# Optimization experiments

Hardware: AMD Instinct MI355X
Metric: run time of the kernel (lower is better)

Reference implementation:

```python
import jax, jax.numpy as jnp
import numpy as np

NUM_HEADS = 12
HEAD_SIZE = 64
HIDDEN = NUM_HEADS * HEAD_SIZE  # 768
ONE_SIDED_WINDOW = 256          # attention_window 512 // 2
NEG = -10000.0


def setup_inputs() -> dict:
    key = jax.random.key(0)
    ks = jax.random.split(key, 16)
    B, W, E, H = 1, 2048, 128, HIDDEN
    std = 0.02
    def lin(kw, kb):
        return (jax.random.normal(kw, (H, H), jnp.float32) * std,
                jax.random.normal(kb, (H,), jnp.float32) * std)
    q_w, q_b = lin(ks[0], ks[1])
    k_w, k_b = lin(ks[2], ks[3])
    v_w, v_b = lin(ks[4], ks[5])
    w2e_w, w2e_b = lin(ks[6], ks[7])
    e2w_w, e2w_b = lin(ks[8], ks[9])
    e2e_w, e2e_b = lin(ks[10], ks[11])
    return {
        "word_hidden_states": jax.random.normal(ks[12], (B, W, H), jnp.float32),
        "entity_hidden_states": jax.random.normal(ks[13], (B, E, H), jnp.float32),
        "attention_mask": jnp.zeros((B, 1, 1, W + E), jnp.float32),
        "q_w": q_w, "q_b": q_b, "k_w": k_w, "k_b": k_b, "v_w": v_w, "v_b": v_b,
        "w2e_w": w2e_w, "w2e_b": w2e_b, "e2w_w": e2w_w, "e2w_b": e2w_b,
        "e2e_w": e2e_w, "e2e_b": e2e_b,
    }


def reference(word_hidden_states, entity_hidden_states, attention_mask,
              q_w, q_b, k_w, k_b, v_w, v_b,
              w2e_w, w2e_b, e2w_w, e2w_b, e2e_w, e2e_b):
    B, W, H = word_hidden_states.shape
    E = entity_hidden_states.shape[1]
    S = W + E

    def heads(x):  # [B, L, H] -> [B, nh, L, hd]
        return x.reshape(B, -1, NUM_HEADS, HEAD_SIZE).transpose(0, 2, 1, 3)

    concat = jnp.concatenate([word_hidden_states, entity_hidden_states], axis=1)
    k = heads(concat @ k_w + k_b)          # [B, nh, S, hd]
    v = heads(concat @ v_w + v_b)
    q_w2w = heads(word_hidden_states @ q_w + q_b)
    q_w2e = heads(word_hidden_states @ w2e_w + w2e_b)
    q_e2w = heads(entity_hidden_states @ e2w_w + e2w_b)
    q_e2e = heads(entity_hidden_states @ e2e_w + e2e_b)

    k_word, k_ent = k[:, :, :W], k[:, :, W:]

    # --- w2w: Longformer sliding-window QK^T, then _conversion to a dense
    # [B, nh, W, W] matrix with out-of-band entries set to -10000. ---
    w2w = jnp.einsum('bhid,bhjd->bhij', q_w2w, k_word)  # [B, nh, W, W]
    idx = jnp.arange(W)
    in_band = jnp.abs(idx[:, None] - idx[None, :]) <= ONE_SIDED_WINDOW  # [W, W]
    # diagonal mask: float_mask[j] (-10000 where attention_mask != 0) added
    # within the band (broadcast over heads / query positions)
    mask_words = attention_mask[:, 0, 0, :W]                # [B, W]
    float_mask = jnp.where(mask_words != 0.0, NEG, 0.0)     # [B, W]
    w2w = w2w + float_mask[:, None, None, :]
    # _conversion: out-of-band -> -10000; also exact zeros -> -10000 (source quirk)
    w2w = jnp.where(in_band[None, None] & (w2w != 0.0), w2w, NEG)

    # --- entity-aware dense blocks ---
    w2e = jnp.einsum('bhid,bhjd->bhij', q_w2e, k_ent)    # [B, nh, W, E]
    e2w = jnp.einsum('bhid,bhjd->bhij', q_e2w, k_word)   # [B, nh, E, W]
    e2e = jnp.einsum('bhid,bhjd->bhij', q_e2e, k_ent)    # [B, nh, E, E]

    word_scores = jnp.concatenate([w2w, w2e], axis=3)    # [B, nh, W, S]
    ent_scores = jnp.concatenate([e2w, e2e], axis=3)     # [B, nh, E, S]
    scores = jnp.concatenate([word_scores, ent_scores], axis=2)  # [B, nh, S, S]

    scores = scores / jnp.sqrt(jnp.float32(HEAD_SIZE)) + attention_mask
    probs = jax.nn.softmax(scores, axis=-1)

    ctx = jnp.einsum('bhij,bhjd->bhid', probs, v)        # [B, nh, S, hd]
    ctx = ctx.transpose(0, 2, 1, 3).reshape(B, S, H)
    return ctx[:, :W, :], ctx[:, W:, :]
```

## Files before the change

kernel.cpp:

```cpp
#include <hip/hip_runtime.h>

typedef __bf16 bf16x8 __attribute__((ext_vector_type(8)));
typedef unsigned short u16x8 __attribute__((ext_vector_type(8)));
typedef u16x8 u16x8_a __attribute__((may_alias));
typedef unsigned int u32x2 __attribute__((ext_vector_type(2)));
typedef u32x2 u32x2_a __attribute__((may_alias));
typedef unsigned int u32x4 __attribute__((ext_vector_type(4)));
typedef u32x4 u32x4_a __attribute__((may_alias));
typedef float f32x4 __attribute__((ext_vector_type(4)));

#define LOG2E 1.4426950408889634f
#define NEGV  -10000.0f

__device__ __forceinline__ unsigned short f2bf(float f){
  union{float f; unsigned int i;} x; x.f=f;
  unsigned int i = x.i;
  return (unsigned short)((i + 0x7FFFu + ((i>>16)&1u)) >> 16);
}
__device__ __forceinline__ u16x8 cvt8(float4 a, float4 b){
  u16x8 r;
  r[0]=f2bf(a.x); r[1]=f2bf(a.y); r[2]=f2bf(a.z); r[3]=f2bf(a.w);
  r[4]=f2bf(b.x); r[5]=f2bf(b.y); r[6]=f2bf(b.z); r[7]=f2bf(b.w);
  return r;
}
__device__ __forceinline__ bf16x8 ldb(const unsigned short* p){
  return __builtin_bit_cast(bf16x8, *(const u16x8_a*)p);
}
__device__ __forceinline__ void gload16(const unsigned short* g, unsigned short* l){
  __builtin_amdgcn_global_load_lds(
    (const __attribute__((address_space(1))) void*)g,
    (__attribute__((address_space(3))) void*)l, 16, 0, 0);
}

__global__ __launch_bounds__(256) void cast_a(
    const float* __restrict__ word, const float* __restrict__ ent,
    unsigned short* __restrict__ Abf)
{
  size_t e = ((size_t)blockIdx.x*256 + threadIdx.x)*8;
  const size_t WE = (size_t)2048*768;
  const float* s = (e < WE) ? (word + e) : (ent + (e - WE));
  float4 a = *(const float4*)s;
  float4 b = *(const float4*)(s+4);
  *(u16x8_a*)(Abf + e) = cvt8(a,b);
}

__global__ __launch_bounds__(256) void transpose6(
    const float* __restrict__ w0, const float* __restrict__ w1,
    const float* __restrict__ w2, const float* __restrict__ w3,
    const float* __restrict__ w4, const float* __restrict__ w5,
    unsigned short* __restrict__ outT)
{
  const float* src;
  switch (blockIdx.z){
    case 0: src = w0; break; case 1: src = w1; break; case 2: src = w2; break;
    case 3: src = w3; break; case 4: src = w4; break; default: src = w5; break;
  }
  unsigned short* dst = outT + (size_t)blockIdx.z * 589824;
  __shared__ float tile[32][33];
  int tx = threadIdx.x, ty = threadIdx.y;
  int x0 = blockIdx.x*32, y0 = blockIdx.y*32;
  #pragma unroll
  for (int i=0;i<32;i+=8) tile[ty+i][tx] = src[(size_t)(y0+ty+i)*768 + x0+tx];
  __syncthreads();
  #pragma unroll
  for (int i=0;i<32;i+=8) dst[(size_t)(x0+ty+i)*768 + y0+tx] = f2bf(tile[tx][ty+i]);
}

__global__ __launch_bounds__(256) void transpose_v(
    const unsigned short* __restrict__ Vb, unsigned short* __restrict__ VbT)
{
  __shared__ unsigned short t[32][33];
  int tx = threadIdx.x, ty = threadIdx.y;
  int x0 = blockIdx.x*32;
  int y0 = blockIdx.y*32;
  #pragma unroll
  for (int i=0;i<32;i+=8) t[ty+i][tx] = Vb[(size_t)(x0+ty+i)*768 + y0+tx];
  __syncthreads();
  #pragma unroll
  for (int i=0;i<32;i+=8) VbT[(size_t)(y0+ty+i)*2176 + x0+tx] = t[tx][ty+i];
}

__global__ __launch_bounds__(256) void gemm_proj(
    const unsigned short* __restrict__ Abf,
    const unsigned short* __restrict__ wT,
    const float* __restrict__ bK, const float* __restrict__ bV,
    const float* __restrict__ bQ, const float* __restrict__ bWE,
    const float* __restrict__ bEW, const float* __restrict__ bEE,
    unsigned short* __restrict__ oK, unsigned short* __restrict__ oV,
    unsigned short* __restrict__ oQ, unsigned short* __restrict__ oWE,
    unsigned short* __restrict__ oEW, unsigned short* __restrict__ oEE)
{
  int mt = blockIdx.x, ntile = blockIdx.y;
  int g, mg;
  if      (mt <  34){ g=0; mg=mt;     }
  else if (mt <  68){ g=1; mg=mt-34;  }
  else if (mt < 100){ g=2; mg=mt-68;  }
  else if (mt < 132){ g=3; mg=mt-100; }
  else if (mt < 134){ g=4; mg=mt-132; }
  else              { g=5; mg=mt-134; }
  int m0 = mg*64;
  const unsigned short* A = Abf + (size_t)((g>=4 ? 2048 : 0) + m0)*768;
  const unsigned short* B = wT + (size_t)g*589824;
  const float* bias; unsigned short* out;
  switch (g){
    case 0: bias=bK;  out=oK;  break;
    case 1: bias=bV;  out=oV;  break;
    case 2: bias=bQ;  out=oQ;  break;
    case 3: bias=bWE; out=oWE; break;
    case 4: bias=bEW; out=oEW; break;
    default:bias=bEE; out=oEE; break;
  }
  out += (size_t)m0*768;
  int n0 = ntile*128;

  __shared__ __align__(16) unsigned short a_s[64*32];
  __shared__ __align__(16) unsigned short b_s[128*32];

  int tid  = threadIdx.x;
  int w    = tid>>6, lane = tid&63, quad = lane>>4, lr = lane&15;
  int wm   = (w&1)*32, wn = (w>>1)*64;

  f32x4 acc[2][4];
  #pragma unroll
  for (int i=0;i<2;i++) for (int j=0;j<4;j++) for (int r=0;r<4;r++) acc[i][j][r]=0.f;

  int srow = lane>>2;
  int scol = (lane&3)*8;
  const unsigned short* gA  = A + (size_t)(w*16 + srow)*768 + scol;
  const unsigned short* gB0 = B + (size_t)(n0 + w*32 + srow)*768 + scol;
  const unsigned short* gB1 = gB0 + (size_t)16*768;
  unsigned short* lA  = a_s + w*16*32;
  unsigned short* lB0 = b_s + w*32*32;
  unsigned short* lB1 = b_s + w*32*32 + 16*32;

  for (int k0=0; k0<768; k0+=32){
    __syncthreads();
    gload16(gA  + k0, lA);
    gload16(gB0 + k0, lB0);
    gload16(gB1 + k0, lB1);
    __syncthreads();
    bf16x8 af[2], bfr[4];
    #pragma unroll
    for (int i=0;i<2;i++) af[i]  = ldb(a_s + (wm+i*16+lr)*32 + quad*8);
    #pragma unroll
    for (int j=0;j<4;j++) bfr[j] = ldb(b_s + (wn+j*16+lr)*32 + quad*8);
    #pragma unroll
    for (int i=0;i<2;i++)
      #pragma unroll
      for (int j=0;j<4;j++)
        acc[i][j] = __builtin_amdgcn_mfma_f32_16x16x32_bf16(af[i], bfr[j], acc[i][j], 0,0,0);
  }
  #pragma unroll
  for (int j=0;j<4;j++){
    int col = n0 + wn + j*16 + lr;
    float bb = bias[col];
    #pragma unroll
    for (int i=0;i<2;i++){
      int rowb = wm + i*16 + quad*4;
      #pragma unroll
      for (int r=0;r<4;r++)
        out[(size_t)(rowb+r)*768 + col] = f2bf(acc[i][j][r] + bb);
    }
  }
}

__global__ __launch_bounds__(256) void attn_split(
  const unsigned short* __restrict__ Kb,  const unsigned short* __restrict__ VbT,
  const unsigned short* __restrict__ Qw,  const unsigned short* __restrict__ Qwe,
  const unsigned short* __restrict__ Qew, const unsigned short* __restrict__ Qee,
  const float* __restrict__ am,
  float* __restrict__ outw, float* __restrict__ pO, float* __restrict__ pML)
{
  int lin = blockIdx.x + 80*blockIdx.y;
  int wid = (lin & 7)*120 + (lin >> 3);
  int bx = wid % 80;
  int h  = wid / 80;

  int tid = threadIdx.x, w = tid>>6, lane = tid&63, quad = lane>>4, lr = lane&15;
  bool isword = bx < 64;
  int qrb, kh, nsplit, eg=0, ehalf=0;
  const unsigned short *Qa, *Qb;
  if (isword){ qrb = bx*32 + (w>>1)*16; kh = w&1; nsplit = 2; Qa=Qw;  Qb=Qwe; }
  else       { int e = bx-64; eg = e>>1; ehalf = e&1;
               qrb = eg*16;             kh = w;   nsplit = 4; Qa=Qew; Qb=Qee; }
  int hofs = h*64;

  __shared__ __align__(16) unsigned int shb[4*64*21];
  unsigned int* p32w = shb + w*(16*44);

  const unsigned short* qr = Qa + (size_t)(qrb+lr)*768 + hofs + quad*8;
  bf16x8 qa0 = ldb(qr), qa1 = ldb(qr + 32);
  qr = Qb + (size_t)(qrb+lr)*768 + hofs + quad*8;
  bf16x8 qb0 = ldb(qr), qb1 = ldb(qr + 32);

  u16x8 onesu;
  #pragma unroll
  for (int i=0;i<8;i++) onesu[i] = 0x3F80;
  bf16x8 onesf = __builtin_bit_cast(bf16x8, onesu);

  float m = -1e30f;
  f32x4 o[4], l4;
  #pragma unroll
  for (int r=0;r<4;r++) l4[r] = 0.f;
  #pragma unroll
  for (int n2=0;n2<4;n2++) for (int r=0;r<4;r++) o[n2][r] = 0.f;

  int lo, nw, start, end, step;
  if (isword){
    lo = qrb - 256; if (lo < 0) lo = 0; lo &= ~31;
    int hi = qrb + 272; if (hi > 2048) hi = 2048; hi = (hi + 31) & ~31;
    nw = (hi - lo) >> 5;
    start = kh; end = nw + 4; step = 2;
  } else {
    lo = 0; nw = 64;
    start = ehalf*34 + kh; end = ehalf*34 + 34; step = 4;
  }
  int iq = qrb + lr;

  for (int c = start; c < end; c += 2*step){
    int c2r = c + step;
    bool ph = (c2r >= end);
    int c2 = ph ? c : c2r;

    bool entp1 = c  >= nw;  int j1 = entp1 ? (2048 + (c -nw)*32) : (lo + c *32);
    bool entp2 = c2 >= nw;  int j2 = entp2 ? (2048 + (c2-nw)*32) : (lo + c2*32);

    const unsigned short* kp1 = Kb + (size_t)(j1+lr)*768 + hofs + quad*8;
    bf16x8 kA0 = ldb(kp1),          kA1 = ldb(kp1 + 32);
    bf16x8 kA2 = ldb(kp1 + 16*768), kA3 = ldb(kp1 + 16*768 + 32);
    const unsigned short* kp2 = Kb + (size_t)(j2+lr)*768 + hofs + quad*8;
    bf16x8 kB0 = ldb(kp2),          kB1 = ldb(kp2 + 32);
    bf16x8 kB2 = ldb(kp2 + 16*768), kB3 = ldb(kp2 + 16*768 + 32);
    const unsigned short* vp1 = VbT + (size_t)(hofs + lr)*2176 + j1 + quad*8;
    bf16x8 v10 = ldb(vp1), v11 = ldb(vp1 + 16*2176), v12 = ldb(vp1 + 32*2176), v13 = ldb(vp1 + 48*2176);
    float4 amA0 = *(const float4*)(am + j1 + quad*4);
    float4 amA1 = *(const float4*)(am + j1 + 16 + quad*4);
    float4 amB0 = *(const float4*)(am + j2 + quad*4);
    float4 amB1 = *(const float4*)(am + j2 + 16 + quad*4);

    bf16x8 qf10 = entp1 ? qb0 : qa0, qf11 = entp1 ? qb1 : qa1;
    bf16x8 qf20 = entp2 ? qb0 : qa0, qf21 = entp2 ? qb1 : qa1;

    f32x4 sA0 = {0.f,0.f,0.f,0.f}, sA1 = {0.f,0.f,0.f,0.f};
    f32x4 sB0 = {0.f,0.f,0.f,0.f}, sB1 = {0.f,0.f,0.f,0.f};
    __builtin_amdgcn_s_setprio(1);
    sA0 = __builtin_amdgcn_mfma_f32_16x16x32_bf16(kA0, qf10, sA0, 0,0,0);
    sA0 = __builtin_amdgcn_mfma_f32_16x16x32_bf16(kA1, qf11, sA0, 0,0,0);
    sA1 = __builtin_amdgcn_mfma_f32_16x16x32_bf16(kA2, qf10, sA1, 0,0,0);
    sA1 = __builtin_amdgcn_mfma_f32_16x16x32_bf16(kA3, qf11, sA1, 0,0,0);
    sB0 = __builtin_amdgcn_mfma_f32_16x16x32_bf16(kB0, qf20, sB0, 0,0,0);
    sB0 = __builtin_amdgcn_mfma_f32_16x16x32_bf16(kB1, qf21, sB0, 0,0,0);
    sB1 = __builtin_amdgcn_mfma_f32_16x16x32_bf16(kB2, qf20, sB1, 0,0,0);
    sB1 = __builtin_amdgcn_mfma_f32_16x16x32_bf16(kB3, qf21, sB1, 0,0,0);
    __builtin_amdgcn_s_setprio(0);

    float scA0[4], scA1[4], scB0[4], scB1[4];
    bool wb1 = isword && !entp1;
    bool wb2 = isword && !entp2;
    #pragma unroll
    for (int r=0;r<4;r++){
      { float amj = amA0[r], sv = sA0[r];
        if (wb1){ sv += (amj != 0.f) ? NEGV : 0.f;
          int j = j1 + quad*4 + r;
          bool ok = ((unsigned)(iq - j + 256) <= 512u) && (sv != 0.f);
          sv = ok ? sv : NEGV; }
        scA0[r] = sv * (LOG2E*0.125f) + amj * LOG2E; }
      { float amj = amA1[r], sv = sA1[r];
        if (wb1){ sv += (amj != 0.f) ? NEGV : 0.f;
          int j = j1 + 16 + quad*4 + r;
          bool ok = ((unsigned)(iq - j + 256) <= 512u) && (sv != 0.f);
          sv = ok ? sv : NEGV; }
        scA1[r] = sv * (LOG2E*0.125f) + amj * LOG2E; }
      { float amj = amB0[r], sv = sB0[r];
        if (wb2){ sv += (amj != 0.f) ? NEGV : 0.f;
          int j = j2 + quad*4 + r;
          bool ok = ((unsigned)(iq - j + 256) <= 512u) && (sv != 0.f);
          sv = ok ? sv : NEGV; }
        scB0[r] = sv * (LOG2E*0.125f) + amj * LOG2E; }
      { float amj = amB1[r], sv = sB1[r];
        if (wb2){ sv += (amj != 0.f) ? NEGV : 0.f;
          int j = j2 + 16 + quad*4 + r;
          bool ok = ((unsigned)(iq - j + 256) <= 512u) && (sv != 0.f);
          sv = ok ? sv : NEGV; }
        scB1[r] = sv * (LOG2E*0.125f) + amj * LOG2E; }
    }
    if (ph){
      #pragma unroll
      for (int r=0;r<4;r++){ scB0[r] = -1e30f; scB1[r] = -1e30f; }
    }

    float mx = fmaxf(
      fmaxf(fmaxf(fmaxf(scA0[0],scA0[1]), fmaxf(scA0[2],scA0[3])),
            fmaxf(fmaxf(scA1[0],scA1[1]), fmaxf(scA1[2],scA1[3]))),
      fmaxf(fmaxf(fmaxf(scB0[0],scB0[1]), fmaxf(scB0[2],scB0[3])),
            fmaxf(fmaxf(scB1[0],scB1[1]), fmaxf(scB1[2],scB1[3]))));
    mx = fmaxf(mx, __shfl_xor(mx, 16));
    mx = fmaxf(mx, __shfl_xor(mx, 32));
    float mn = fmaxf(m, mx);
    float alpha = exp2f(m - mn);
    m = mn;

    unsigned int xA0 = (unsigned int)f2bf(exp2f(scA0[0]-mn)) | ((unsigned int)f2bf(exp2f(scA0[1]-mn))<<16);
    unsigned int xA1 = (unsigned int)f2bf(exp2f(scA0[2]-mn)) | ((unsigned int)f2bf(exp2f(scA0[3]-mn))<<16);
    unsigned int xA2 = (unsigned int)f2bf(exp2f(scA1[0]-mn)) | ((unsigned int)f2bf(exp2f(scA1[1]-mn))<<16);
    unsigned int xA3 = (unsigned int)f2bf(exp2f(scA1[2]-mn)) | ((unsigned int)f2bf(exp2f(scA1[3]-mn))<<16);
    unsigned int xB0 = (unsigned int)f2bf(exp2f(scB0[0]-mn)) | ((unsigned int)f2bf(exp2f(scB0[1]-mn))<<16);
    unsigned int xB1 = (unsigned int)f2bf(exp2f(scB0[2]-mn)) | ((unsigned int)f2bf(exp2f(scB0[3]-mn))<<16);
    unsigned int xB2 = (unsigned int)f2bf(exp2f(scB1[0]-mn)) | ((unsigned int)f2bf(exp2f(scB1[1]-mn))<<16);
    unsigned int xB3 = (unsigned int)f2bf(exp2f(scB1[2]-mn)) | ((unsigned int)f2bf(exp2f(scB1[3]-mn))<<16);

    #pragma unroll
    for (int r=0;r<4;r++) l4[r] *= alpha;
    #pragma unroll
    for (int n2=0;n2<4;n2++)
      #pragma unroll
      for (int r=0;r<4;r++) o[n2][r] *= alpha;

    unsigned int* row = p32w + lr*44;
    u32x2 wv0 = {xA0, xA1};
    u32x2 wv1 = {xA2, xA3};
    u32x2 wv2 = {xB0, xB1};
    u32x2 wv3 = {xB2, xB3};
    *(u32x2_a*)(row + quad*2)      = wv0;
    *(u32x2_a*)(row + 8  + quad*2) = wv1;
    *(u32x2_a*)(row + 16 + quad*2) = wv2;
    *(u32x2_a*)(row + 24 + quad*2) = wv3;
    bf16x8 pf1 = ldb((const unsigned short*)(p32w + lr*44 + quad*4));
    bf16x8 pf2 = ldb((const unsigned short*)(p32w + lr*44 + 16 + quad*4));

    __builtin_amdgcn_s_setprio(1);
    o[0] = __builtin_amdgcn_mfma_f32_16x16x32_bf16(v10, pf1, o[0], 0,0,0);
    o[1] = __builtin_amdgcn_mfma_f32_16x16x32_bf16(v11, pf1, o[1], 0,0,0);
    o[2] = __builtin_amdgcn_mfma_f32_16x16x32_bf16(v12, pf1, o[2], 0,0,0);
    o[3] = __builtin_amdgcn_mfma_f32_16x16x32_bf16(v13, pf1, o[3], 0,0,0);
    l4   = __builtin_amdgcn_mfma_f32_16x16x32_bf16(onesf, pf1, l4, 0,0,0);
    __builtin_amdgcn_s_setprio(0);

    const unsigned short* vp2 = VbT + (size_t)(hofs + lr)*2176 + j2 + quad*8;
    bf16x8 v20 = ldb(vp2), v21 = ldb(vp2 + 16*2176), v22 = ldb(vp2 + 32*2176), v23 = ldb(vp2 + 48*2176);

    __builtin_amdgcn_s_setprio(1);
    o[0] = __builtin_amdgcn_mfma_f32_16x16x32_bf16(v20, pf2, o[0], 0,0,0);
    o[1] = __builtin_amdgcn_mfma_f32_16x16x32_bf16(v21, pf2, o[1], 0,0,0);
    o[2] = __builtin_amdgcn_mfma_f32_16x16x32_bf16(v22, pf2, o[2], 0,0,0);
    o[3] = __builtin_amdgcn_mfma_f32_16x16x32_bf16(v23, pf2, o[3], 0,0,0);
    l4   = __builtin_amdgcn_mfma_f32_16x16x32_bf16(onesf, pf2, l4, 0,0,0);
    __builtin_amdgcn_s_setprio(0);
  }

  float lsc = l4[0];
  __syncthreads();
  {
    float* my = (float*)shb + ((size_t)(w*64 + lane))*21;
    my[0] = m; my[1] = lsc;
    #pragma unroll
    for (int n2=0;n2<4;n2++)
      #pragma unroll
      for (int r=0;r<4;r++) my[2+n2*4+r] = o[n2][r];
  }
  __syncthreads();
  if (kh == 0){
    for (int p=1; p<nsplit; p++){
      const float* pr = (float*)shb + ((size_t)((w+p)*64 + lane))*21;
      float m2 = pr[0], l2 = pr[1];
      float M  = fmaxf(m, m2);
      float e1 = exp2f(m-M), e2 = exp2f(m2-M);
      m = M;
      lsc = lsc*e1 + l2*e2;
      #pragma unroll
      for (int n2=0;n2<4;n2++)
        #pragma unroll
        for (int r=0;r<4;r++)
          o[n2][r] = o[n2][r]*e1 + pr[2+n2*4+r]*e2;
    }
    if (isword){
      float rinv = 1.f / lsc;
      #pragma unroll
      for (int n2=0;n2<4;n2++){
        float4 sv;
        sv.x = o[n2][0]*rinv; sv.y = o[n2][1]*rinv;
        sv.z = o[n2][2]*rinv; sv.w = o[n2][3]*rinv;
        *(float4*)(outw + (size_t)(qrb+lr)*768 + hofs + n2*16 + quad*4) = sv;
      }
    } else {
      int idx = (eg*12 + h)*2 + ehalf;
      float* po = pO + (size_t)idx*1024;
      #pragma unroll
      for (int n2=0;n2<4;n2++){
        float4 sv;
        sv.x = o[n2][0]; sv.y = o[n2][1]; sv.z = o[n2][2]; sv.w = o[n2][3];
        *(float4*)(po + lr*64 + n2*16 + quad*4) = sv;
      }
      if (quad == 0){
        float* pml = pML + (size_t)idx*32;
        pml[lr*2]     = m;
        pml[lr*2 + 1] = lsc;
      }
    }
  }
}

__global__ __launch_bounds__(256) void merge_ent(
    const float* __restrict__ pO, const float* __restrict__ pML,
    float* __restrict__ oute)
{
  int b = blockIdx.x;
  int g = b/12, h = b%12;
  int tid = threadIdx.x;
  int row = tid>>4, cg = tid&15;
  int i0 = b*2, i1 = b*2+1;
  float m0 = pML[(size_t)i0*32 + row*2], l0 = pML[(size_t)i0*32 + row*2 + 1];
  float m1 = pML[(size_t)i1*32 + row*2], l1 = pML[(size_t)i1*32 + row*2 + 1];
  float M  = fmaxf(m0, m1);
  float e0 = exp2f(m0-M), e1 = exp2f(m1-M);
  float rl = 1.f/(l0*e0 + l1*e1);
  float4 a = *(const float4*)(pO + (size_t)i0*1024 + row*64 + cg*4);
  float4 c = *(const float4*)(pO + (size_t)i1*1024 + row*64 + cg*4);
  float4 o;
  o.x = (a.x*e0 + c.x*e1)*rl;
  o.y = (a.y*e0 + c.y*e1)*rl;
  o.z = (a.z*e0 + c.z*e1)*rl;
  o.w = (a.w*e0 + c.w*e1)*rl;
  *(float4*)(oute + (size_t)(g*16+row)*768 + h*64 + cg*4) = o;
}

extern "C" void kernel_launch(void* const* d_in, const int* in_sizes, int n_in,
                              void* d_out, int out_size, void* d_ws, size_t ws_size,
                              hipStream_t stream) {
  const float* word  = (const float*)d_in[0];
  const float* ent   = (const float*)d_in[1];
  const float* am    = (const float*)d_in[2];
  const float* q_w   = (const float*)d_in[3];
  const float* q_b   = (const float*)d_in[4];
  const float* k_w   = (const float*)d_in[5];
  const float* k_b   = (const float*)d_in[6];
  const float* v_w   = (const float*)d_in[7];
  const float* v_b   = (const float*)d_in[8];
  const float* w2e_w = (const float*)d_in[9];
  const float* w2e_b = (const float*)d_in[10];
  const float* e2w_w = (const float*)d_in[11];
  const float* e2w_b = (const float*)d_in[12];
  const float* e2e_w = (const float*)d_in[13];
  const float* e2e_b = (const float*)d_in[14];

  unsigned short* ws  = (unsigned short*)d_ws;
  unsigned short* wT  = ws;
  unsigned short* Kb  = wT  + (size_t)6*589824;
  unsigned short* Vb  = Kb  + (size_t)2176*768;
  unsigned short* Qw  = Vb  + (size_t)2176*768;
  unsigned short* Qwe = Qw  + (size_t)2048*768;
  unsigned short* Qew = Qwe + (size_t)2048*768;
  unsigned short* Qee = Qew + (size_t)128*768;
  unsigned short* VbT = Qee + (size_t)128*768;
  unsigned short* Abf = VbT + (size_t)768*2176;

  float* pO  = (float*)wT;
  float* pML = pO + (size_t)192*1024;

  float* outw = (float*)d_out;
  float* oute = outw + (size_t)2048*768;

  hipLaunchKernelGGL(cast_a, dim3(816), dim3(256), 0, stream, word, ent, Abf);
  hipLaunchKernelGGL(transpose6, dim3(24,24,6), dim3(32,8), 0, stream,
                     k_w, v_w, q_w, w2e_w, e2w_w, e2e_w, wT);
  hipLaunchKernelGGL(gemm_proj, dim3(136,6), dim3(256), 0, stream,
                     Abf, wT, k_b, v_b, q_b, w2e_b, e2w_b, e2e_b,
                     Kb, Vb, Qw, Qwe, Qew, Qee);
  hipLaunchKernelGGL(transpose_v, dim3(68,24), dim3(32,8), 0, stream, Vb, VbT);
  hipLaunchKernelGGL(attn_split, dim3(80,12), dim3(256), 0, stream,
                     Kb, VbT, Qw, Qwe, Qew, Qee, am, outw, pO, pML);
  hipLaunchKernelGGL(merge_ent, dim3(96), dim3(256), 0, stream,
                     pO, pML, oute);
}
```

Measured before the change: 172.8 us.

## Merge prep kernels, fuse V transpose into GEMM epilogue, enlarge GEMM tile

The weight-transpose, input cast and mask preprocessing move into one prep kernel, which cuts launches. The projection GEMM now uses 128x128 tiles, and its V epilogue writes the transposed layout directly, so the separate transpose_v kernel is gone. In the attention loop, the online-softmax rescale is skipped when no row max changes, the mask is precomputed into scaled and penalty arrays, and bf16 packing uses the hardware v_cvt_pk_bf16_f32 instruction. Risks are fewer GEMM blocks (408 versus 816), which lowers occupancy, and strided 8-byte transposed stores in the epilogue.

```diff
diff --git a/kernel.cpp b/kernel.cpp
--- a/kernel.cpp
+++ b/kernel.cpp
@@ -12,15 +12,9 @@
 #define LOG2E 1.4426950408889634f
 #define NEGV  -10000.0f
 
-__device__ __forceinline__ unsigned short f2bf(float f){
-  union{float f; unsigned int i;} x; x.f=f;
-  unsigned int i = x.i;
-  return (unsigned short)((i + 0x7FFFu + ((i>>16)&1u)) >> 16);
-}
-__device__ __forceinline__ u16x8 cvt8(float4 a, float4 b){
-  u16x8 r;
-  r[0]=f2bf(a.x); r[1]=f2bf(a.y); r[2]=f2bf(a.z); r[3]=f2bf(a.w);
-  r[4]=f2bf(b.x); r[5]=f2bf(b.y); r[6]=f2bf(b.z); r[7]=f2bf(b.w);
+__device__ __forceinline__ unsigned int cvtpk(float lo, float hi){
+  unsigned int r;
+  asm("v_cvt_pk_bf16_f32 %0, %1, %2" : "=v"(r) : "v"(lo), "v"(hi));
   return r;
 }
 __device__ __forceinline__ bf16x8 ldb(const unsigned short* p){
@@ -32,52 +26,56 @@
     (__attribute__((address_space(3))) void*)l, 16, 0, 0);
 }
 
-__global__ __launch_bounds__(256) void cast_a(
-    const float* __restrict__ word, const float* __restrict__ ent,
-    unsigned short* __restrict__ Abf)
-{
-  size_t e = ((size_t)blockIdx.x*256 + threadIdx.x)*8;
-  const size_t WE = (size_t)2048*768;
-  const float* s = (e < WE) ? (word + e) : (ent + (e - WE));
-  float4 a = *(const float4*)s;
-  float4 b = *(const float4*)(s+4);
-  *(u16x8_a*)(Abf + e) = cvt8(a,b);
-}
-
-__global__ __launch_bounds__(256) void transpose6(
+__global__ __launch_bounds__(256) void prep(
     const float* __restrict__ w0, const float* __restrict__ w1,
     const float* __restrict__ w2, const float* __restrict__ w3,
     const float* __restrict__ w4, const float* __restrict__ w5,
-    unsigned short* __restrict__ outT)
+    const float* __restrict__ word, const float* __restrict__ ent,
+    const float* __restrict__ am,
+    unsigned short* __restrict__ outT, unsigned short* __restrict__ Abf,
+    float* __restrict__ amT, float* __restrict__ negT)
 {
+  int z = blockIdx.z, tid = threadIdx.x;
+  if (z == 6){
+    size_t id = (size_t)blockIdx.y*24 + blockIdx.x;
+    size_t e = (id*256 + tid)*8;
+    const size_t WE = (size_t)2048*768;
+    const float* s = (e < WE) ? (word + e) : (ent + (e - WE));
+    float4 a = *(const float4*)s;
+    float4 b = *(const float4*)(s+4);
+    u32x4 v = {cvtpk(a.x,a.y), cvtpk(a.z,a.w), cvtpk(b.x,b.y), cvtpk(b.z,b.w)};
+    *(u32x4_a*)(Abf + e) = v;
+    return;
+  }
+  if (z == 7){
+    if (blockIdx.y != 0 || blockIdx.x >= 9) return;
+    int j = blockIdx.x*256 + tid;
+    if (j < 2176){
+      float a = am[j];
+      amT[j]  = a * LOG2E;
+      negT[j] = (a != 0.f) ? NEGV : 0.f;
+    }
+    return;
+  }
+  if (blockIdx.y >= 24) return;
   const float* src;
-  switch (blockIdx.z){
+  switch (z){
     case 0: src = w0; break; case 1: src = w1; break; case 2: src = w2; break;
     case 3: src = w3; break; case 4: src = w4; break; default: src = w5; break;
   }
-  unsigned short* dst = outT + (size_t)blockIdx.z * 589824;
+  unsigned short* dst = outT + (size_t)z * 589824;
   __shared__ float tile[32][33];
-  int tx = threadIdx.x, ty = threadIdx.y;
+  int tx = tid & 31, ty = tid >> 5;
   int x0 = blockIdx.x*32, y0 = blockIdx.y*32;
   #pragma unroll
   for (int i=0;i<32;i+=8) tile[ty+i][tx] = src[(size_t)(y0+ty+i)*768 + x0+tx];
   __syncthreads();
   #pragma unroll
-  for (int i=0;i<32;i+=8) dst[(size_t)(x0+ty+i)*768 + y0+tx] = f2bf(tile[tx][ty+i]);
-}
-
-__global__ __launch_bounds__(256) void transpose_v(
-    const unsigned short* __restrict__ Vb, unsigned short* __restrict__ VbT)
-{
-  __shared__ unsigned short t[32][33];
-  int tx = threadIdx.x, ty = threadIdx.y;
-  int x0 = blockIdx.x*32;
-  int y0 = blockIdx.y*32;
-  #pragma unroll
-  for (int i=0;i<32;i+=8) t[ty+i][tx] = Vb[(size_t)(x0+ty+i)*768 + y0+tx];
-  __syncthreads();
-  #pragma unroll
-  for (int i=0;i<32;i+=8) VbT[(size_t)(y0+ty+i)*2176 + x0+tx] = t[tx][ty+i];
+  for (int i=0;i<32;i+=16){
+    unsigned int u = cvtpk(tile[tx][ty+i], tile[tx][ty+i+8]);
+    dst[(size_t)(x0+ty+i)*768 + y0+tx]   = (unsigned short)u;
+    dst[(size_t)(x0+ty+i+8)*768 + y0+tx] = (unsigned short)(u>>16);
+  }
 }
 
 __global__ __launch_bounds__(256) void gemm_proj(
@@ -86,80 +84,101 @@
     const float* __restrict__ bK, const float* __restrict__ bV,
     const float* __restrict__ bQ, const float* __restrict__ bWE,
     const float* __restrict__ bEW, const float* __restrict__ bEE,
-    unsigned short* __restrict__ oK, unsigned short* __restrict__ oV,
+    unsigned short* __restrict__ oK, unsigned short* __restrict__ VbT,
     unsigned short* __restrict__ oQ, unsigned short* __restrict__ oWE,
     unsigned short* __restrict__ oEW, unsigned short* __restrict__ oEE)
 {
   int mt = blockIdx.x, ntile = blockIdx.y;
   int g, mg;
-  if      (mt <  34){ g=0; mg=mt;     }
-  else if (mt <  68){ g=1; mg=mt-34;  }
-  else if (mt < 100){ g=2; mg=mt-68;  }
-  else if (mt < 132){ g=3; mg=mt-100; }
-  else if (mt < 134){ g=4; mg=mt-132; }
-  else              { g=5; mg=mt-134; }
-  int m0 = mg*64;
+  if      (mt < 17){ g=0; mg=mt;    }
+  else if (mt < 34){ g=1; mg=mt-17; }
+  else if (mt < 50){ g=2; mg=mt-34; }
+  else if (mt < 66){ g=3; mg=mt-50; }
+  else if (mt < 67){ g=4; mg=0;     }
+  else             { g=5; mg=0;     }
+  int m0 = mg*128;
   const unsigned short* A = Abf + (size_t)((g>=4 ? 2048 : 0) + m0)*768;
   const unsigned short* B = wT + (size_t)g*589824;
   const float* bias; unsigned short* out;
   switch (g){
     case 0: bias=bK;  out=oK;  break;
-    case 1: bias=bV;  out=oV;  break;
+    case 1: bias=bV;  out=0;   break;
     case 2: bias=bQ;  out=oQ;  break;
     case 3: bias=bWE; out=oWE; break;
     case 4: bias=bEW; out=oEW; break;
     default:bias=bEE; out=oEE; break;
   }
-  out += (size_t)m0*768;
   int n0 = ntile*128;
 
-  __shared__ __align__(16) unsigned short a_s[64*32];
+  __shared__ __align__(16) unsigned short a_s[128*32];
   __shared__ __align__(16) unsigned short b_s[128*32];
 
   int tid  = threadIdx.x;
   int w    = tid>>6, lane = tid&63, quad = lane>>4, lr = lane&15;
-  int wm   = (w&1)*32, wn = (w>>1)*64;
-
-  f32x4 acc[2][4];
+  int wm   = (w&1)*64, wn = (w>>1)*64;
+
+  f32x4 acc[4][4];
   #pragma unroll
-  for (int i=0;i<2;i++) for (int j=0;j<4;j++) for (int r=0;r<4;r++) acc[i][j][r]=0.f;
+  for (int i=0;i<4;i++) for (int j=0;j<4;j++) for (int r=0;r<4;r++) acc[i][j][r]=0.f;
 
   int srow = lane>>2;
   int scol = (lane&3)*8;
-  const unsigned short* gA  = A + (size_t)(w*16 + srow)*768 + scol;
+  const unsigned short* gA0 = A + (size_t)(w*32 + srow)*768 + scol;
+  const unsigned short* gA1 = gA0 + (size_t)16*768;
   const unsigned short* gB0 = B + (size_t)(n0 + w*32 + srow)*768 + scol;
   const unsigned short* gB1 = gB0 + (size_t)16*768;
-  unsigned short* lA  = a_s + w*16*32;
+  unsigned short* lA0 = a_s + w*32*32;
+  unsigned short* lA1 = lA0 + 16*32;
   unsigned short* lB0 = b_s + w*32*32;
-  unsigned short* lB1 = b_s + w*32*32 + 16*32;
+  unsigned short* lB1 = lB0 + 16*32;
 
   for (int k0=0; k0<768; k0+=32){
     __syncthreads();
-    gload16(gA  + k0, lA);
+    gload16(gA0 + k0, lA0);
+    gload16(gA1 + k0, lA1);
     gload16(gB0 + k0, lB0);
     gload16(gB1 + k0, lB1);
     __syncthreads();
-    bf16x8 af[2], bfr[4];
-    #pragma unroll
-    for (int i=0;i<2;i++) af[i]  = ldb(a_s + (wm+i*16+lr)*32 + quad*8);
+    bf16x8 af[4], bfr[4];
+    #pragma unroll
+    for (int i=0;i<4;i++) af[i]  = ldb(a_s + (wm+i*16+lr)*32 + quad*8);
     #pragma unroll
     for (int j=0;j<4;j++) bfr[j] = ldb(b_s + (wn+j*16+lr)*32 + quad*8);
     #pragma unroll
-    for (int i=0;i<2;i++)
+    for (int i=0;i<4;i++)
       #pragma unroll
       for (int j=0;j<4;j++)
         acc[i][j] = __builtin_amdgcn_mfma_f32_16x16x32_bf16(af[i], bfr[j], acc[i][j], 0,0,0);
   }
-  #pragma unroll
-  for (int j=0;j<4;j++){
-    int col = n0 + wn + j*16 + lr;
-    float bb = bias[col];
-    #pragma unroll
-    for (int i=0;i<2;i++){
-      int rowb = wm + i*16 + quad*4;
-      #pragma unroll
-      for (int r=0;r<4;r++)
-        out[(size_t)(rowb+r)*768 + col] = f2bf(acc[i][j][r] + bb);
+  if (g == 1){
+    #pragma unroll
+    for (int j=0;j<4;j++){
+      int col = n0 + wn + j*16 + lr;
+      float bb = bias[col];
+      #pragma unroll
+      for (int i=0;i<4;i++){
+        int rowb = m0 + wm + i*16 + quad*4;
+        u32x2 uv = {cvtpk(acc[i][j][0]+bb, acc[i][j][1]+bb),
+                    cvtpk(acc[i][j][2]+bb, acc[i][j][3]+bb)};
+        *(u32x2_a*)(VbT + (size_t)col*2176 + rowb) = uv;
+      }
+    }
+  } else {
+    out += (size_t)m0*768;
+    #pragma unroll
+    for (int j=0;j<4;j++){
+      int col = n0 + wn + j*16 + lr;
+      float bb = bias[col];
+      #pragma unroll
+      for (int i=0;i<4;i++){
+        int rowb = wm + i*16 + quad*4;
+        unsigned int u01 = cvtpk(acc[i][j][0]+bb, acc[i][j][1]+bb);
+        unsigned int u23 = cvtpk(acc[i][j][2]+bb, acc[i][j][3]+bb);
+        out[(size_t)(rowb+0)*768 + col] = (unsigned short)u01;
+        out[(size_t)(rowb+1)*768 + col] = (unsigned short)(u01>>16);
+        out[(size_t)(rowb+2)*768 + col] = (unsigned short)u23;
+        out[(size_t)(rowb+3)*768 + col] = (unsigned short)(u23>>16);
+      }
     }
   }
 }
@@ -168,7 +187,7 @@
   const unsigned short* __restrict__ Kb,  const unsigned short* __restrict__ VbT,
   const unsigned short* __restrict__ Qw,  const unsigned short* __restrict__ Qwe,
   const unsigned short* __restrict__ Qew, const unsigned short* __restrict__ Qee,
-  const float* __restrict__ am,
+  const float* __restrict__ amT, const float* __restrict__ negT,
   float* __restrict__ outw, float* __restrict__ pO, float* __restrict__ pML)
 {
   int lin = blockIdx.x + 80*blockIdx.y;
@@ -233,10 +252,14 @@
     bf16x8 kB2 = ldb(kp2 + 16*768), kB3 = ldb(kp2 + 16*768 + 32);
     const unsigned short* vp1 = VbT + (size_t)(hofs + lr)*2176 + j1 + quad*8;
     bf16x8 v10 = ldb(vp1), v11 = ldb(vp1 + 16*2176), v12 = ldb(vp1 + 32*2176), v13 = ldb(vp1 + 48*2176);
-    float4 amA0 = *(const float4*)(am + j1 + quad*4);
-    float4 amA1 = *(const float4*)(am + j1 + 16 + quad*4);
-    float4 amB0 = *(const float4*)(am + j2 + quad*4);
-    float4 amB1 = *(const float4*)(am + j2 + 16 + quad*4);
+    float4 aA0 = *(const float4*)(amT + j1 + quad*4);
+    float4 aA1 = *(const float4*)(amT + j1 + 16 + quad*4);
+    float4 aB0 = *(const float4*)(amT + j2 + quad*4);
+    float4 aB1 = *(const float4*)(amT + j2 + 16 + quad*4);
+    float4 nA0 = *(const float4*)(negT + j1 + quad*4);
+    float4 nA1 = *(const float4*)(negT + j1 + 16 + quad*4);
+    float4 nB0 = *(const float4*)(negT + j2 + quad*4);
+    float4 nB1 = *(const float4*)(negT + j2 + 16 + quad*4);
 
     bf16x8 qf10 = entp1 ? qb0 : qa0, qf11 = entp1 ? qb1 : qa1;
     bf16x8 qf20 = entp2 ? qb0 : qa0, qf21 = entp2 ? qb1 : qa1;
@@ -259,30 +282,30 @@
     bool wb2 = isword && !entp2;
     #pragma unroll
     for (int r=0;r<4;r++){
-      { float amj = amA0[r], sv = sA0[r];
-        if (wb1){ sv += (amj != 0.f) ? NEGV : 0.f;
+      { float sv = sA0[r];
+        if (wb1){ sv += nA0[r];
           int j = j1 + quad*4 + r;
           bool ok = ((unsigned)(iq - j + 256) <= 512u) && (sv != 0.f);
           sv = ok ? sv : NEGV; }
-        scA0[r] = sv * (LOG2E*0.125f) + amj * LOG2E; }
-      { float amj = amA1[r], sv = sA1[r];
-        if (wb1){ sv += (amj != 0.f) ? NEGV : 0.f;
+        scA0[r] = sv * (LOG2E*0.125f) + aA0[r]; }
+      { float sv = sA1[r];
+        if (wb1){ sv += nA1[r];
           int j = j1 + 16 + quad*4 + r;
           bool ok = ((unsigned)(iq - j + 256) <= 512u) && (sv != 0.f);
           sv = ok ? sv : NEGV; }
-        scA1[r] = sv * (LOG2E*0.125f) + amj * LOG2E; }
-      { float amj = amB0[r], sv = sB0[r];
-        if (wb2){ sv += (amj != 0.f) ? NEGV : 0.f;
+        scA1[r] = sv * (LOG2E*0.125f) + aA1[r]; }
+      { float sv = sB0[r];
+        if (wb2){ sv += nB0[r];
           int j = j2 + quad*4 + r;
           bool ok = ((unsigned)(iq - j + 256) <= 512u) && (sv != 0.f);
           sv = ok ? sv : NEGV; }
-        scB0[r] = sv * (LOG2E*0.125f) + amj * LOG2E; }
-      { float amj = amB1[r], sv = sB1[r];
-        if (wb2){ sv += (amj != 0.f) ? NEGV : 0.f;
+        scB0[r] = sv * (LOG2E*0.125f) + aB0[r]; }
+      { float sv = sB1[r];
+        if (wb2){ sv += nB1[r];
           int j = j2 + 16 + quad*4 + r;
           bool ok = ((unsigned)(iq - j + 256) <= 512u) && (sv != 0.f);
           sv = ok ? sv : NEGV; }
-        scB1[r] = sv * (LOG2E*0.125f) + amj * LOG2E; }
+        scB1[r] = sv * (LOG2E*0.125f) + aB1[r]; }
     }
     if (ph){
       #pragma unroll
@@ -296,25 +319,30 @@
             fmaxf(fmaxf(scB1[0],scB1[1]), fmaxf(scB1[2],scB1[3]))));
     mx = fmaxf(mx, __shfl_xor(mx, 16));
     mx = fmaxf(mx, __shfl_xor(mx, 32));
-    float mn = fmaxf(m, mx);
-    float alpha = exp2f(m - mn);
-    m = mn;
-
-    unsigned int xA0 = (unsigned int)f2bf(exp2f(scA0[0]-mn)) | ((unsigned int)f2bf(exp2f(scA0[1]-mn))<<16);
-    unsigned int xA1 = (unsigned int)f2bf(exp2f(scA0[2]-mn)) | ((unsigned int)f2bf(exp2f(scA0[3]-mn))<<16);
-    unsigned int xA2 = (unsigned int)f2bf(exp2f(scA1[0]-mn)) | ((unsigned int)f2bf(exp2f(scA1[1]-mn))<<16);
-    unsigned int xA3 = (unsigned int)f2bf(exp2f(scA1[2]-mn)) | ((unsigned int)f2bf(exp2f(scA1[3]-mn))<<16);
-    unsigned int xB0 = (unsigned int)f2bf(exp2f(scB0[0]-mn)) | ((unsigned int)f2bf(exp2f(scB0[1]-mn))<<16);
-    unsigned int xB1 = (unsigned int)f2bf(exp2f(scB0[2]-mn)) | ((unsigned int)f2bf(exp2f(scB0[3]-mn))<<16);
-    unsigned int xB2 = (unsigned int)f2bf(exp2f(scB1[0]-mn)) | ((unsigned int)f2bf(exp2f(scB1[1]-mn))<<16);
-    unsigned int xB3 = (unsigned int)f2bf(exp2f(scB1[2]-mn)) | ((unsigned int)f2bf(exp2f(scB1[3]-mn))<<16);
-
-    #pragma unroll
-    for (int r=0;r<4;r++) l4[r] *= alpha;
-    #pragma unroll
-    for (int n2=0;n2<4;n2++)
-      #pragma unroll
-      for (int r=0;r<4;r++) o[n2][r] *= alpha;
+
+    float mn;
+    if (__all(mx <= m)){
+      mn = m;
+    } else {
+      mn = fmaxf(m, mx);
+      float alpha = exp2f(m - mn);
+      m = mn;
+      #pragma unroll
+      for (int r=0;r<4;r++) l4[r] *= alpha;
+      #pragma unroll
+      for (int n2=0;n2<4;n2++)
+        #pragma unroll
+        for (int r=0;r<4;r++) o[n2][r] *= alpha;
+    }
+
+    unsigned int xA0 = cvtpk(exp2f(scA0[0]-mn), exp2f(scA0[1]-mn));
+    unsigned int xA1 = cvtpk(exp2f(scA0[2]-mn), exp2f(scA0[3]-mn));
+    unsigned int xA2 = cvtpk(exp2f(scA1[0]-mn), exp2f(scA1[1]-mn));
+    unsigned int xA3 = cvtpk(exp2f(scA1[2]-mn), exp2f(scA1[3]-mn));
+    unsigned int xB0 = cvtpk(exp2f(scB0[0]-mn), exp2f(scB0[1]-mn));
+    unsigned int xB1 = cvtpk(exp2f(scB0[2]-mn), exp2f(scB0[3]-mn));
+    unsigned int xB2 = cvtpk(exp2f(scB1[0]-mn), exp2f(scB1[1]-mn));
+    unsigned int xB3 = cvtpk(exp2f(scB1[2]-mn), exp2f(scB1[3]-mn));
 
     unsigned int* row = p32w + lr*44;
     u32x2 wv0 = {xA0, xA1};
@@ -446,29 +474,31 @@
   unsigned short* ws  = (unsigned short*)d_ws;
   unsigned short* wT  = ws;
   unsigned short* Kb  = wT  + (size_t)6*589824;
-  unsigned short* Vb  = Kb  + (size_t)2176*768;
-  unsigned short* Qw  = Vb  + (size_t)2176*768;
+  unsigned short* Tb  = Kb  + (size_t)2176*768;
+  unsigned short* Qw  = Tb  + (size_t)2176*768;
   unsigned short* Qwe = Qw  + (size_t)2048*768;
   unsigned short* Qew = Qwe + (size_t)2048*768;
   unsigned short* Qee = Qew + (size_t)128*768;
   unsigned short* VbT = Qee + (size_t)128*768;
   unsigned short* Abf = VbT + (size_t)768*2176;
 
+  float* amT  = (float*)Tb;
+  float* negT = amT + 2176;
+
   float* pO  = (float*)wT;
   float* pML = pO + (size_t)192*1024;
 
   float* outw = (float*)d_out;
   float* oute = outw + (size_t)2048*768;
 
-  hipLaunchKernelGGL(cast_a, dim3(816), dim3(256), 0, stream, word, ent, Abf);
-  hipLaunchKernelGGL(transpose6, dim3(24,24,6), dim3(32,8), 0, stream,
-                     k_w, v_w, q_w, w2e_w, e2w_w, e2e_w, wT);
-  hipLaunchKernelGGL(gemm_proj, dim3(136,6), dim3(256), 0, stream,
+  hipLaunchKernelGGL(prep, dim3(24,34,8), dim3(256), 0, stream,
+                     k_w, v_w, q_w, w2e_w, e2w_w, e2e_w, word, ent, am,
+                     wT, Abf, amT, negT);
+  hipLaunchKernelGGL(gemm_proj, dim3(68,6), dim3(256), 0, stream,
                      Abf, wT, k_b, v_b, q_b, w2e_b, e2w_b, e2e_b,
-                     Kb, Vb, Qw, Qwe, Qew, Qee);
-  hipLaunchKernelGGL(transpose_v, dim3(68,24), dim3(32,8), 0, stream, Vb, VbT);
+                     Kb, VbT, Qw, Qwe, Qew, Qee);
   hipLaunchKernelGGL(attn_split, dim3(80,12), dim3(256), 0, stream,
-                     Kb, VbT, Qw, Qwe, Qew, Qee, am, outw, pO, pML);
+                     Kb, VbT, Qw, Qwe, Qew, Qee, amT, negT, outw, pO, pML);
   hipLaunchKernelGGL(merge_ent, dim3(96), dim3(256), 0, stream,
                      pO, pML, oute);
 }
```

New measurement: 169.4 us. No clear change (-1.9%).
